# Optimization experiments

Hardware: AMD Instinct MI355X
Metric: run time of the kernel (lower is better)

Reference implementation:

```python
import jax, jax.numpy as jnp
import numpy as np
from jax import lax

B, CIN, COUT, K, SDIM, H = 8, 512, 512, 3, 512, 32
EPS = 1e-8
LRELU_SLOPE = 0.2
ACT_SCALE = float(np.sqrt(2.0))


def setup_inputs() -> dict:
    key = jax.random.key(0)
    k1, k2, k3, k4 = jax.random.split(key, 4)
    return {
        "x": jax.random.normal(k1, (B, CIN, H, H), jnp.float32),
        "style": jax.random.normal(k2, (B, SDIM), jnp.float32),
        "weight": jax.random.normal(k3, (COUT, CIN, K, K), jnp.float32),
        "mod_w": jax.random.normal(k4, (CIN, SDIM), jnp.float32),
        "mod_b": jnp.ones((CIN,), jnp.float32),  # EqualLinear bias_init=1
        "bias": jnp.zeros((COUT,), jnp.float32),  # FusedLeakyReLU bias
    }


def _blur_kernel(c):
    bk = np.array([1.0, 3.0, 3.0, 1.0], np.float32)
    bk = bk[None, :] * bk[:, None]
    bk = bk / bk.sum() * 4.0  # upsample_factor ** 2
    return jnp.tile(jnp.asarray(bk)[None, None], (c, 1, 1, 1))  # (C,1,4,4)


def reference(x, style, weight, mod_w, mod_b, bias):
    b, cin, h, w = x.shape
    cout, k = weight.shape[0], weight.shape[-1]
    conv_scale = 1.0 / np.sqrt(cin * k * k)
    lin_scale = 1.0 / np.sqrt(mod_w.shape[1])

    # style modulation: EqualLinear(style_dim -> in_channel), bias_init=1
    s = style @ (mod_w * lin_scale).T + mod_b  # (B, Cin)

    # per-sample modulated weights (B, Cout, Cin, k, k)
    wmod = conv_scale * weight[None] * s[:, None, :, None, None]
    demod = lax.rsqrt(jnp.sum(wmod * wmod, axis=(2, 3, 4)) + EPS)
    wmod = wmod * demod[:, :, None, None, None]

    # conv_transpose2d(stride=2, pad=0) == conv with lhs_dilation=2, pad=k-1,
    # spatially-flipped kernel (torch transposes (Cout,Cin)->(Cin,Cout)).
    wflip = jnp.flip(wmod, (-2, -1))

    def convt(xi, wi):  # xi: (Cin,H,W), wi: (Cout,Cin,k,k)
        return lax.conv_general_dilated(
            xi[None], wi, (1, 1), [(k - 1, k - 1)] * 2,
            lhs_dilation=(2, 2),
            dimension_numbers=("NCHW", "OIHW", "NCHW"))[0]

    y = jax.vmap(convt)(x, wflip)  # (B, Cout, 2H+1, 2W+1)

    # Blur: upfirdn2d with pad=(1,1), depthwise 4x4 FIR (kernel symmetric)
    bk = _blur_kernel(cout)
    y = lax.conv_general_dilated(
        y, bk, (1, 1), [(1, 1), (1, 1)],
        feature_group_count=cout,
        dimension_numbers=("NCHW", "OIHW", "NCHW"))  # (B, Cout, 2H, 2W)

    # FusedLeakyReLU: leaky_relu(y + bias) * sqrt(2)
    z = y + bias[None, :, None, None]
    return jnp.where(z >= 0, z, LRELU_SLOPE * z) * ACT_SCALE
```

## Files before the change

kernel.cpp:

```cpp
#include <hip/hip_runtime.h>
#include <hip/hip_bf16.h>

#define NB 8
#define CIN 512
#define COUT 512
#define SDIM 512

typedef __attribute__((ext_vector_type(8))) short short8;
typedef __attribute__((ext_vector_type(4))) float f32x4;

static constexpr float CONV_SCALE = 0.014731391274719740f;
static constexpr float LIN_SCALE  = 0.044194173824159216f;

static constexpr size_t OFF_S     = 0;
static constexpr size_t OFF_WSQ   = 16384;
static constexpr size_t OFF_DEMOD = 1064960;
static constexpr size_t OFF_XP    = 1081344;
static constexpr size_t OFF_WP    = 10551296;
static constexpr size_t OFF_Y1    = 15269888;
static constexpr size_t XP_BYTES  = 9469952;

static constexpr int NJOBS = 1060;

__device__ __forceinline__ int wpoff(int ps) {
  return ps == 0 ? 0 : ps == 1 ? 1048576 : ps == 2 ? 1572864 : 2097152;
}
__device__ __forceinline__ constexpr int y1off(int ps) {
  return ps == 0 ? 0 : ps == 1 ? 4460544 : ps == 2 ? 8785920 : 13111296;
}

__device__ __forceinline__ short f2bf(float f) {
  unsigned u = __builtin_bit_cast(unsigned, f);
  unsigned r = (u + 0x7fffu + ((u >> 16) & 1u)) >> 16;
  return (short)r;
}
__device__ __forceinline__ float bf2f(unsigned short u) {
  return __builtin_bit_cast(float, (unsigned)u << 16);
}

__device__ __forceinline__ void load_lds16(const short* g, short* l) {
  __builtin_amdgcn_global_load_lds(
      (const __attribute__((address_space(1))) unsigned int*)g,
      (__attribute__((address_space(3))) unsigned int*)l, 16, 0, 0);
}

__global__ void k_prep1(const float* __restrict__ style, const float* __restrict__ mod_w,
                        const float* __restrict__ mod_b, float* __restrict__ s_out,
                        const float* __restrict__ w, short* __restrict__ wp,
                        float* __restrict__ wsq) {
  const int tid = threadIdx.x;
  if (blockIdx.x < 1024) {
    int idx = blockIdx.x * 256 + tid;
    int co = idx >> 9, ci = idx & 511;
    float wv[3][3];
    float sq = 0.f;
#pragma unroll
    for (int i = 0; i < 9; ++i) {
      float v = w[idx * 9 + i];
      wv[i / 3][i % 3] = v;
      sq += v * v;
    }
    wsq[idx] = sq * CONV_SCALE * CONV_SCALE;
#pragma unroll
    for (int wy = 0; wy < 3; ++wy)
#pragma unroll
      for (int wx = 0; wx < 3; ++wx) {
        int psy = (wy == 1) ? 1 : 0, psx = (wx == 1) ? 1 : 0;
        int u = psy ? 0 : (wy == 0 ? 1 : 0);
        int v = psx ? 0 : (wx == 0 ? 1 : 0);
        int ps = psy * 2 + psx;
        int tap = psy ? (psx ? 0 : v) : (psx ? u : u * 2 + v);
        int k = tap * 512 + ci;
        int elem = wpoff(ps) + ((k >> 6) * 512 + co) * 64 + (k & 63);
        wp[elem] = f2bf(wv[wy][wx] * CONV_SCALE);
      }
  } else {
    int wid = tid >> 6, lane = tid & 63;
    int ci = (blockIdx.x - 1024) * 4 + wid;
    float acc[NB] = {};
    for (int k = lane; k < SDIM; k += 64) {
      float wm = mod_w[ci * SDIM + k];
#pragma unroll
      for (int b = 0; b < NB; ++b) acc[b] += wm * style[b * SDIM + k];
    }
#pragma unroll
    for (int b = 0; b < NB; ++b) {
      float v = acc[b];
      for (int o = 32; o > 0; o >>= 1) v += __shfl_xor(v, o);
      if (lane == 0) s_out[b * CIN + ci] = v * LIN_SCALE + mod_b[ci];
    }
  }
}

__global__ void k_prep2(const float* __restrict__ wsq, const float* __restrict__ s,
                        float* __restrict__ demod,
                        const float* __restrict__ x, short* __restrict__ xp) {
  const int tid = threadIdx.x;
  if (blockIdx.x < 1024) {
    __shared__ float t[64][65];
    const int tx = tid & 63, ty = tid >> 6;
    int bx = blockIdx.x;
    int sp0 = (bx & 15) * 64, ci0 = ((bx >> 4) & 7) * 64, b = bx >> 7;
    for (int r = ty; r < 64; r += 4)
      t[r][tx] = x[(b * CIN + ci0 + r) * 1024 + sp0 + tx];
    __syncthreads();
    int ci = ci0 + tx;
    float sv = s[b * CIN + ci];
    for (int r = ty; r < 64; r += 4) {
      int sp = sp0 + r;
      int yy = sp >> 5, xx = sp & 31;
      xp[((b * 34 + yy + 1) * 34 + (xx + 1)) * 512 + ci] = f2bf(t[tx][r] * sv);
    }
  } else {
    int wid = tid >> 6, lane = tid & 63;
    int co = (blockIdx.x - 1024) * 4 + wid;
    float acc[NB] = {};
    for (int ci = lane; ci < CIN; ci += 64) {
      float wq = wsq[co * CIN + ci];
#pragma unroll
      for (int b = 0; b < NB; ++b) {
        float sv = s[b * CIN + ci];
        acc[b] += wq * sv * sv;
      }
    }
#pragma unroll
    for (int b = 0; b < NB; ++b) {
      float v = acc[b];
      for (int o = 32; o > 0; o >>= 1) v += __shfl_xor(v, o);
      if (lane == 0) demod[b * COUT + co] = rsqrtf(v + 1e-8f);
    }
  }
}

#define MFMA_ROWPAIR(AH, AL, RH, RL)                                              \
  __builtin_amdgcn_s_setprio(1);                                                  \
  acc[RH][0] = __builtin_amdgcn_mfma_f32_16x16x32_bf16(AH, b0, acc[RH][0], 0,0,0);\
  acc[RH][1] = __builtin_amdgcn_mfma_f32_16x16x32_bf16(AH, b1, acc[RH][1], 0,0,0);\
  acc[RH][2] = __builtin_amdgcn_mfma_f32_16x16x32_bf16(AH, b2, acc[RH][2], 0,0,0);\
  acc[RH][3] = __builtin_amdgcn_mfma_f32_16x16x32_bf16(AH, b3, acc[RH][3], 0,0,0);\
  acc[RL][0] = __builtin_amdgcn_mfma_f32_16x16x32_bf16(AL, b0, acc[RL][0], 0,0,0);\
  acc[RL][1] = __builtin_amdgcn_mfma_f32_16x16x32_bf16(AL, b1, acc[RL][1], 0,0,0);\
  acc[RL][2] = __builtin_amdgcn_mfma_f32_16x16x32_bf16(AL, b2, acc[RL][2], 0,0,0);\
  acc[RL][3] = __builtin_amdgcn_mfma_f32_16x16x32_bf16(AL, b3, acc[RL][3], 0,0,0);\
  __builtin_amdgcn_s_setprio(0);

__global__ __launch_bounds__(256, 2) void k_gemm(const short* __restrict__ xp,
                                                 const short* __restrict__ wp,
                                                 short* __restrict__ y1) {
  __shared__ short sW[2][128 * 64];
  __shared__ short sX[2][128 * 64];

  const int tid = threadIdx.x;
  const int wid = tid >> 6, lane = tid & 63;
  const int hi = lane >> 4;
  const int ksw8 = ((tid & 7) ^ ((tid >> 3) & 7)) * 8;
  const int wm = (wid >> 1) * 64, wn = (wid & 1) * 64;

  const int bx = blockIdx.x;
  const int xcd = bx & 7, ii = bx >> 3;
  const int j = (((ii >> 2) << 3) + xcd) * 4 + (ii & 3);
  if (j >= NJOBS) return;

  int ps, base;
  if (j < 276)      { ps = 0; base = 0; }
  else if (j < 540) { ps = 1; base = 276; }
  else if (j < 804) { ps = 2; base = 540; }
  else              { ps = 3; base = 804; }
  const int r = j - base;
  const int nb = r >> 2, mb = r & 3;
  const int psy = ps >> 1, psx = ps & 1;
  const int Ny = 33 - psy, Nx = 33 - psx;
  const int N = NB * Ny * Nx;
  const int n0 = nb * 128, m0 = mb * 128;
  const int KT = (2 - psy) * (2 - psx) * 8;
  const short* wpb = wp + wpoff(ps);
  short* y1b = y1 + y1off(ps);

  int bb[4], ay[4], ax[4];
#pragma unroll
  for (int i = 0; i < 4; ++i) {
    int seg = i * 256 + tid;
    int n = n0 + (seg >> 3);
    if (n >= N) n = N - 1;
    int b = n / (Ny * Nx);
    int rem = n - b * (Ny * Nx);
    int a_y = rem / Nx;
    bb[i] = b; ay[i] = a_y; ax[i] = rem - a_y * Nx;
  }

  auto STAGE = [&](int kt, int d) {
    int tap = kt >> 3, ci0 = (kt & 7) << 6;
    int oy, ox;
    if (ps == 0)      { oy = tap >> 1; ox = tap & 1; }
    else if (ps == 1) { oy = tap;      ox = 1; }
    else if (ps == 2) { oy = 1;        ox = tap; }
    else              { oy = 1;        ox = 1; }
#pragma unroll
    for (int i = 0; i < 4; ++i) {
      int seg = i * 256 + tid;
      const short* gw = wpb + (kt * 512 + m0 + (seg >> 3)) * 64 + ksw8;
      load_lds16(gw, &sW[d][(i * 4 + wid) * 512]);
    }
#pragma unroll
    for (int i = 0; i < 4; ++i) {
      const short* gx = xp + ((bb[i] * 34 + ay[i] + oy) * 34 + ax[i] + ox) * 512 + ci0 + ksw8;
      load_lds16(gx, &sX[d][(i * 4 + wid) * 512]);
    }
  };

  const int c0 = ((hi)     ^ (lane & 7)) * 8;
  const int c1 = ((4 + hi) ^ (lane & 7)) * 8;
  const int rA0 = (wm +  0 + (lane & 15)) * 64, rA1 = (wm + 16 + (lane & 15)) * 64;
  const int rA2 = (wm + 32 + (lane & 15)) * 64, rA3 = (wm + 48 + (lane & 15)) * 64;
  const int rB0 = (wn +  0 + (lane & 15)) * 64, rB1 = (wn + 16 + (lane & 15)) * 64;
  const int rB2 = (wn + 32 + (lane & 15)) * 64, rB3 = (wn + 48 + (lane & 15)) * 64;

  f32x4 acc[4][4] = {};

  STAGE(0, 0);
  STAGE(1, 1);
  __syncthreads();

  int cur = 0;
  for (int t = 0; t < KT; ++t) {
    const short* W = sW[cur];
    const short* X = sX[cur];
    short8 a0, a1, b0, b1, b2, b3;

    a0 = *(const short8*)&W[rA0 + c0];
    a1 = *(const short8*)&W[rA1 + c0];
    b0 = *(const short8*)&X[rB0 + c0];
    b1 = *(const short8*)&X[rB1 + c0];
    b2 = *(const short8*)&X[rB2 + c0];
    b3 = *(const short8*)&X[rB3 + c0];
    MFMA_ROWPAIR(a0, a1, 0, 1);
    __builtin_amdgcn_s_barrier();

    a0 = *(const short8*)&W[rA2 + c0];
    a1 = *(const short8*)&W[rA3 + c0];
    MFMA_ROWPAIR(a0, a1, 2, 3);
    __builtin_amdgcn_s_barrier();

    a0 = *(const short8*)&W[rA0 + c1];
    a1 = *(const short8*)&W[rA1 + c1];
    b0 = *(const short8*)&X[rB0 + c1];
    b1 = *(const short8*)&X[rB1 + c1];
    b2 = *(const short8*)&X[rB2 + c1];
    b3 = *(const short8*)&X[rB3 + c1];
    MFMA_ROWPAIR(a0, a1, 0, 1);
    __builtin_amdgcn_s_barrier();

    a0 = *(const short8*)&W[rA2 + c1];
    a1 = *(const short8*)&W[rA3 + c1];
    MFMA_ROWPAIR(a0, a1, 2, 3);

    __syncthreads();
    if (t + 2 < KT) STAGE(t + 2, cur);
    cur ^= 1;
  }

#pragma unroll
  for (int mf = 0; mf < 4; ++mf) {
    int m = m0 + wm + mf * 16 + (lane >> 4) * 4;
#pragma unroll
    for (int nf = 0; nf < 4; ++nf) {
      int n = n0 + wn + nf * 16 + (lane & 15);
      if (n < N) {
#pragma unroll
        for (int rr = 0; rr < 4; ++rr) y1b[(m + rr) * N + n] = f2bf(acc[mf][nf][rr]);
      }
    }
  }
}

__global__ __launch_bounds__(256, 4) void k_blur(const short* __restrict__ y1,
                                                 const float* __restrict__ demod,
                                                 const float* __restrict__ bias,
                                                 float* __restrict__ out) {
  __shared__ float sin_[4][35 * 35];
  __shared__ float stmp[2][35][64];
  const int tid = threadIdx.x;
  const int bc = blockIdx.x;
  const int co = bc & 511, b = bc >> 9;

  for (int i = tid; i < 4 * 35 * 35; i += 256) ((float*)sin_)[i] = 0.f;
  __syncthreads();

#pragma unroll
  for (int ps = 0; ps < 4; ++ps) {
    const int Nyv = 33 - (ps >> 1), Nxv = 33 - (ps & 1);
    const short* pl = y1 + y1off(ps) + (co * NB + b) * (Nyv * Nxv);
    for (int t = tid; t < Nyv * Nxv; t += 256) {
      int av = t / Nxv, ah = t - av * Nxv;
      sin_[ps][(av + 1) * 35 + ah + 1] = bf2f((unsigned short)pl[t]);
    }
  }
  __syncthreads();

  const int q = tid & 63;
  const int mx = q >> 1, fx = q & 1;
  int xp0, xi0, xp1, xi1, xp2, xi2, xp3, xi3;
  if (fx) { xp0 = 0; xi0 = mx + 1; xp1 = 1; xi1 = mx + 1; xp2 = 0; xi2 = mx + 2; xp3 = 1; xi3 = mx + 2; }
  else    { xp0 = 1; xi0 = mx;     xp1 = 0; xi1 = mx + 1; xp2 = 1; xi2 = mx + 1; xp3 = 0; xi3 = mx + 2; }

  for (int r = tid >> 6; r < 70; r += 4) {
    int pv = (r >= 35) ? 1 : 0;
    int av = r - pv * 35;
    float v = 0.25f * sin_[pv * 2 + xp0][av * 35 + xi0]
            + 0.75f * sin_[pv * 2 + xp1][av * 35 + xi1]
            + 0.75f * sin_[pv * 2 + xp2][av * 35 + xi2]
            + 0.25f * sin_[pv * 2 + xp3][av * 35 + xi3];
    stmp[pv][av][q] = v;
  }
  __syncthreads();

  const float dm = demod[b * COUT + co], bs = bias[co];
  for (int p = tid >> 6; p < 64; p += 4) {
    int my = p >> 1, fy = p & 1;
    float v;
    if (fy) v = 0.25f * stmp[0][my + 1][q] + 0.75f * stmp[1][my + 1][q]
              + 0.75f * stmp[0][my + 2][q] + 0.25f * stmp[1][my + 2][q];
    else    v = 0.25f * stmp[1][my][q]     + 0.75f * stmp[0][my + 1][q]
              + 0.75f * stmp[1][my + 1][q] + 0.25f * stmp[0][my + 2][q];
    float val = dm * v + bs;
    out[(bc * 64 + p) * 64 + q] = (val >= 0.f ? val : 0.2f * val) * 1.41421356237309515f;
  }
}

extern "C" void kernel_launch(void* const* d_in, const int* in_sizes, int n_in,
                              void* d_out, int out_size, void* d_ws, size_t ws_size,
                              hipStream_t stream) {
  const float* x      = (const float*)d_in[0];
  const float* style  = (const float*)d_in[1];
  const float* weight = (const float*)d_in[2];
  const float* mod_w  = (const float*)d_in[3];
  const float* mod_b  = (const float*)d_in[4];
  const float* bias   = (const float*)d_in[5];
  float* out = (float*)d_out;
  char* ws = (char*)d_ws;

  float* s     = (float*)(ws + OFF_S);
  float* wsq   = (float*)(ws + OFF_WSQ);
  float* demod = (float*)(ws + OFF_DEMOD);
  short* xp    = (short*)(ws + OFF_XP);
  short* wp    = (short*)(ws + OFF_WP);
  short* y1    = (short*)(ws + OFF_Y1);

  hipMemsetAsync(xp, 0, XP_BYTES, stream);
  k_prep1<<<1152, 256, 0, stream>>>(style, mod_w, mod_b, s, weight, wp, wsq);
  k_prep2<<<1152, 256, 0, stream>>>(wsq, s, demod, x, xp);
  k_gemm<<<1088, 256, 0, stream>>>(xp, wp, y1);
  k_blur<<<4096, 256, 0, stream>>>(y1, demod, bias, out);
}
```

Measured before the change: 131.9 us.

## Use 4-stage K32 LDS pipeline in GEMM and zero only padding border

The GEMM main loop moves from a double-buffered K=64 stage to a four-buffer ring of K=32 stages with three tiles in flight. Explicit vmcnt waits and a single barrier pair per step replace the previous multiple barriers, and the LDS swizzle changes to match. Separately, the full memset of the padded input buffer is dropped; extra blocks in prep2 zero only the one-pixel border, since the interior is fully overwritten anyway. This removes a memset launch and bandwidth, but the hand-counted vmcnt values must match the number of loads issued per stage.

```diff
diff --git a/kernel.cpp b/kernel.cpp
--- a/kernel.cpp
+++ b/kernel.cpp
@@ -18,7 +18,6 @@
 static constexpr size_t OFF_XP    = 1081344;
 static constexpr size_t OFF_WP    = 10551296;
 static constexpr size_t OFF_Y1    = 15269888;
-static constexpr size_t XP_BYTES  = 9469952;
 
 static constexpr int NJOBS = 1060;
 
@@ -111,7 +110,7 @@
       int yy = sp >> 5, xx = sp & 31;
       xp[((b * 34 + yy + 1) * 34 + (xx + 1)) * 512 + ci] = f2bf(t[tx][r] * sv);
     }
-  } else {
+  } else if (blockIdx.x < 1152) {
     int wid = tid >> 6, lane = tid & 63;
     int co = (blockIdx.x - 1024) * 4 + wid;
     float acc[NB] = {};
@@ -129,31 +128,31 @@
       for (int o = 32; o > 0; o >>= 1) v += __shfl_xor(v, o);
       if (lane == 0) demod[b * COUT + co] = rsqrtf(v + 1e-8f);
     }
-  }
-}
-
-#define MFMA_ROWPAIR(AH, AL, RH, RL)                                              \
-  __builtin_amdgcn_s_setprio(1);                                                  \
-  acc[RH][0] = __builtin_amdgcn_mfma_f32_16x16x32_bf16(AH, b0, acc[RH][0], 0,0,0);\
-  acc[RH][1] = __builtin_amdgcn_mfma_f32_16x16x32_bf16(AH, b1, acc[RH][1], 0,0,0);\
-  acc[RH][2] = __builtin_amdgcn_mfma_f32_16x16x32_bf16(AH, b2, acc[RH][2], 0,0,0);\
-  acc[RH][3] = __builtin_amdgcn_mfma_f32_16x16x32_bf16(AH, b3, acc[RH][3], 0,0,0);\
-  acc[RL][0] = __builtin_amdgcn_mfma_f32_16x16x32_bf16(AL, b0, acc[RL][0], 0,0,0);\
-  acc[RL][1] = __builtin_amdgcn_mfma_f32_16x16x32_bf16(AL, b1, acc[RL][1], 0,0,0);\
-  acc[RL][2] = __builtin_amdgcn_mfma_f32_16x16x32_bf16(AL, b2, acc[RL][2], 0,0,0);\
-  acc[RL][3] = __builtin_amdgcn_mfma_f32_16x16x32_bf16(AL, b3, acc[RL][3], 0,0,0);\
-  __builtin_amdgcn_s_setprio(0);
+  } else {
+    int idx = blockIdx.x - 1152;
+    int b = idx >> 2, part = idx & 3;
+    unsigned* xpu = (unsigned*)xp;
+    for (int k = 0; k < 33; ++k) {
+      int c = part * 33 + k;
+      int yy, xx;
+      if (c < 34)       { yy = 0;            xx = c; }
+      else if (c < 68)  { yy = 33;           xx = c - 34; }
+      else if (c < 100) { yy = 1 + (c - 68); xx = 0; }
+      else              { yy = 1 + (c - 100); xx = 33; }
+      xpu[((((b * 34 + yy) * 34 + xx) * 512) >> 1) + tid] = 0u;
+    }
+  }
+}
 
 __global__ __launch_bounds__(256, 2) void k_gemm(const short* __restrict__ xp,
                                                  const short* __restrict__ wp,
                                                  short* __restrict__ y1) {
-  __shared__ short sW[2][128 * 64];
-  __shared__ short sX[2][128 * 64];
+  __shared__ short sW[4][128 * 32];
+  __shared__ short sX[4][128 * 32];
 
   const int tid = threadIdx.x;
   const int wid = tid >> 6, lane = tid & 63;
   const int hi = lane >> 4;
-  const int ksw8 = ((tid & 7) ^ ((tid >> 3) & 7)) * 8;
   const int wm = (wid >> 1) * 64, wn = (wid & 1) * 64;
 
   const int bx = blockIdx.x;
@@ -172,91 +171,84 @@
   const int Ny = 33 - psy, Nx = 33 - psx;
   const int N = NB * Ny * Nx;
   const int n0 = nb * 128, m0 = mb * 128;
-  const int KT = (2 - psy) * (2 - psx) * 8;
+  const int KT32 = (2 - psy) * (2 - psx) * 16;
   const short* wpb = wp + wpoff(ps);
   short* y1b = y1 + y1off(ps);
 
-  int bb[4], ay[4], ax[4];
-#pragma unroll
-  for (int i = 0; i < 4; ++i) {
-    int seg = i * 256 + tid;
-    int n = n0 + (seg >> 3);
+  int bb2[2], ay2[2], ax2[2];
+#pragma unroll
+  for (int i = 0; i < 2; ++i) {
+    int n = n0 + i * 64 + (tid >> 2);
     if (n >= N) n = N - 1;
     int b = n / (Ny * Nx);
     int rem = n - b * (Ny * Nx);
     int a_y = rem / Nx;
-    bb[i] = b; ay[i] = a_y; ax[i] = rem - a_y * Nx;
+    bb2[i] = b; ay2[i] = a_y; ax2[i] = rem - a_y * Nx;
   }
 
   auto STAGE = [&](int kt, int d) {
-    int tap = kt >> 3, ci0 = (kt & 7) << 6;
+    int tap = kt >> 4, ci0 = (kt & 15) << 5;
     int oy, ox;
     if (ps == 0)      { oy = tap >> 1; ox = tap & 1; }
     else if (ps == 1) { oy = tap;      ox = 1; }
     else if (ps == 2) { oy = 1;        ox = tap; }
     else              { oy = 1;        ox = 1; }
 #pragma unroll
-    for (int i = 0; i < 4; ++i) {
+    for (int i = 0; i < 2; ++i) {
       int seg = i * 256 + tid;
-      const short* gw = wpb + (kt * 512 + m0 + (seg >> 3)) * 64 + ksw8;
-      load_lds16(gw, &sW[d][(i * 4 + wid) * 512]);
-    }
-#pragma unroll
-    for (int i = 0; i < 4; ++i) {
-      const short* gx = xp + ((bb[i] * 34 + ay[i] + oy) * 34 + ax[i] + ox) * 512 + ci0 + ksw8;
-      load_lds16(gx, &sX[d][(i * 4 + wid) * 512]);
+      int row = seg >> 2;
+      int clog = (seg & 3) ^ ((row >> 1) & 3);
+      const short* gw = wpb + ((kt >> 1) * 512 + m0 + row) * 64 + (kt & 1) * 32 + clog * 8;
+      load_lds16(gw, &sW[d][seg * 8]);
+    }
+#pragma unroll
+    for (int i = 0; i < 2; ++i) {
+      int seg = i * 256 + tid;
+      int row = seg >> 2;
+      int clog = (seg & 3) ^ ((row >> 1) & 3);
+      const short* gx = xp + ((bb2[i] * 34 + ay2[i] + oy) * 34 + ax2[i] + ox) * 512 + ci0 + clog * 8;
+      load_lds16(gx, &sX[d][seg * 8]);
     }
   };
 
-  const int c0 = ((hi)     ^ (lane & 7)) * 8;
-  const int c1 = ((4 + hi) ^ (lane & 7)) * 8;
-  const int rA0 = (wm +  0 + (lane & 15)) * 64, rA1 = (wm + 16 + (lane & 15)) * 64;
-  const int rA2 = (wm + 32 + (lane & 15)) * 64, rA3 = (wm + 48 + (lane & 15)) * 64;
-  const int rB0 = (wn +  0 + (lane & 15)) * 64, rB1 = (wn + 16 + (lane & 15)) * 64;
-  const int rB2 = (wn + 32 + (lane & 15)) * 64, rB3 = (wn + 48 + (lane & 15)) * 64;
+  int offA[4], offB[4];
+#pragma unroll
+  for (int f = 0; f < 4; ++f) {
+    int ra = wm + f * 16 + (lane & 15);
+    offA[f] = ra * 32 + ((hi ^ ((ra >> 1) & 3)) * 8);
+    int rb = wn + f * 16 + (lane & 15);
+    offB[f] = rb * 32 + ((hi ^ ((rb >> 1) & 3)) * 8);
+  }
 
   f32x4 acc[4][4] = {};
 
-  STAGE(0, 0);
-  STAGE(1, 1);
-  __syncthreads();
-
-  int cur = 0;
-  for (int t = 0; t < KT; ++t) {
-    const short* W = sW[cur];
-    const short* X = sX[cur];
-    short8 a0, a1, b0, b1, b2, b3;
-
-    a0 = *(const short8*)&W[rA0 + c0];
-    a1 = *(const short8*)&W[rA1 + c0];
-    b0 = *(const short8*)&X[rB0 + c0];
-    b1 = *(const short8*)&X[rB1 + c0];
-    b2 = *(const short8*)&X[rB2 + c0];
-    b3 = *(const short8*)&X[rB3 + c0];
-    MFMA_ROWPAIR(a0, a1, 0, 1);
+  STAGE(0, 0); STAGE(1, 1); STAGE(2, 2);
+
+  for (int t = 0; t < KT32; ++t) {
+    int rem = KT32 - 1 - t;
+    if (rem >= 2)      asm volatile("s_waitcnt vmcnt(8)" ::: "memory");
+    else if (rem == 1) asm volatile("s_waitcnt vmcnt(4)" ::: "memory");
+    else               asm volatile("s_waitcnt vmcnt(0)" ::: "memory");
     __builtin_amdgcn_s_barrier();
 
-    a0 = *(const short8*)&W[rA2 + c0];
-    a1 = *(const short8*)&W[rA3 + c0];
-    MFMA_ROWPAIR(a0, a1, 2, 3);
+    const short* W = sW[t & 3];
+    const short* X = sX[t & 3];
+    short8 af[4], bf[4];
+#pragma unroll
+    for (int f = 0; f < 4; ++f) af[f] = *(const short8*)&W[offA[f]];
+#pragma unroll
+    for (int f = 0; f < 4; ++f) bf[f] = *(const short8*)&X[offB[f]];
+
+    __builtin_amdgcn_s_setprio(1);
+#pragma unroll
+    for (int mf = 0; mf < 4; ++mf)
+#pragma unroll
+      for (int nf = 0; nf < 4; ++nf)
+        acc[mf][nf] = __builtin_amdgcn_mfma_f32_16x16x32_bf16(af[mf], bf[nf], acc[mf][nf], 0, 0, 0);
+    __builtin_amdgcn_s_setprio(0);
+
     __builtin_amdgcn_s_barrier();
-
-    a0 = *(const short8*)&W[rA0 + c1];
-    a1 = *(const short8*)&W[rA1 + c1];
-    b0 = *(const short8*)&X[rB0 + c1];
-    b1 = *(const short8*)&X[rB1 + c1];
-    b2 = *(const short8*)&X[rB2 + c1];
-    b3 = *(const short8*)&X[rB3 + c1];
-    MFMA_ROWPAIR(a0, a1, 0, 1);
-    __builtin_amdgcn_s_barrier();
-
-    a0 = *(const short8*)&W[rA2 + c1];
-    a1 = *(const short8*)&W[rA3 + c1];
-    MFMA_ROWPAIR(a0, a1, 2, 3);
-
-    __syncthreads();
-    if (t + 2 < KT) STAGE(t + 2, cur);
-    cur ^= 1;
+    if (t + 3 < KT32) STAGE(t + 3, (t + 3) & 3);
   }
 
 #pragma unroll
@@ -346,9 +338,8 @@
   short* wp    = (short*)(ws + OFF_WP);
   short* y1    = (short*)(ws + OFF_Y1);
 
-  hipMemsetAsync(xp, 0, XP_BYTES, stream);
   k_prep1<<<1152, 256, 0, stream>>>(style, mod_w, mod_b, s, weight, wp, wsq);
-  k_prep2<<<1152, 256, 0, stream>>>(wsq, s, demod, x, xp);
+  k_prep2<<<1184, 256, 0, stream>>>(wsq, s, demod, x, xp);
   k_gemm<<<1088, 256, 0, stream>>>(xp, wp, y1);
   k_blur<<<4096, 256, 0, stream>>>(y1, demod, bias, out);
 }
```

Result: slower. 139.9 us (+6.1%).

## Zero only padding border in prep, pad y1 planes, split blur into halves

Applied to the files above, without the earlier changes.

Drops the full memset of the padded x buffer and instead zeroes only the border pixels with extra blocks in k_prep2. Each phase plane of y1 gets an even-padded stride so the blur kernel can load bf16 pairs with 32-bit reads. The blur kernel is split into two row-halves per (b, co), which halves its LDS use and raises occupancy, at the cost of loading overlapping halo rows and filtering out rows it does not need. The GEMM epilogue now computes per-column batch offsets for the padded layout.

```diff
diff --git a/kernel.cpp b/kernel.cpp
--- a/kernel.cpp
+++ b/kernel.cpp
@@ -18,15 +18,17 @@
 static constexpr size_t OFF_XP    = 1081344;
 static constexpr size_t OFF_WP    = 10551296;
 static constexpr size_t OFF_Y1    = 15269888;
-static constexpr size_t XP_BYTES  = 9469952;
 
 static constexpr int NJOBS = 1060;
 
 __device__ __forceinline__ int wpoff(int ps) {
   return ps == 0 ? 0 : ps == 1 ? 1048576 : ps == 2 ? 1572864 : 2097152;
 }
-__device__ __forceinline__ constexpr int y1off(int ps) {
-  return ps == 0 ? 0 : ps == 1 ? 4460544 : ps == 2 ? 8785920 : 13111296;
+__device__ __forceinline__ constexpr int PSPAD(int ps) {
+  return ps == 0 ? 1090 : ps == 3 ? 1024 : 1056;
+}
+__device__ __forceinline__ constexpr int PLB(int ps) {
+  return ps == 0 ? 0 : ps == 1 ? 4464640 : ps == 2 ? 8790016 : 13115392;
 }
 
 __device__ __forceinline__ short f2bf(float f) {
@@ -111,7 +113,7 @@
       int yy = sp >> 5, xx = sp & 31;
       xp[((b * 34 + yy + 1) * 34 + (xx + 1)) * 512 + ci] = f2bf(t[tx][r] * sv);
     }
-  } else {
+  } else if (blockIdx.x < 1152) {
     int wid = tid >> 6, lane = tid & 63;
     int co = (blockIdx.x - 1024) * 4 + wid;
     float acc[NB] = {};
@@ -128,6 +130,19 @@
       float v = acc[b];
       for (int o = 32; o > 0; o >>= 1) v += __shfl_xor(v, o);
       if (lane == 0) demod[b * COUT + co] = rsqrtf(v + 1e-8f);
+    }
+  } else {
+    int idx = blockIdx.x - 1152;
+    int b = idx >> 2, part = idx & 3;
+    unsigned* xpu = (unsigned*)xp;
+    for (int k = 0; k < 33; ++k) {
+      int c = part * 33 + k;
+      int yy, xx;
+      if (c < 34)       { yy = 0;            xx = c; }
+      else if (c < 68)  { yy = 33;           xx = c - 34; }
+      else if (c < 100) { yy = 1 + (c - 68); xx = 0; }
+      else              { yy = 1 + (c - 100); xx = 33; }
+      xpu[((((b * 34 + yy) * 34 + xx) * 512) >> 1) + tid] = 0u;
     }
   }
 }
@@ -170,11 +185,11 @@
   const int nb = r >> 2, mb = r & 3;
   const int psy = ps >> 1, psx = ps & 1;
   const int Ny = 33 - psy, Nx = 33 - psx;
-  const int N = NB * Ny * Nx;
+  const int NyNx = Ny * Nx;
+  const int N = NB * NyNx;
   const int n0 = nb * 128, m0 = mb * 128;
   const int KT = (2 - psy) * (2 - psx) * 8;
   const short* wpb = wp + wpoff(ps);
-  short* y1b = y1 + y1off(ps);
 
   int bb[4], ay[4], ax[4];
 #pragma unroll
@@ -182,8 +197,8 @@
     int seg = i * 256 + tid;
     int n = n0 + (seg >> 3);
     if (n >= N) n = N - 1;
-    int b = n / (Ny * Nx);
-    int rem = n - b * (Ny * Nx);
+    int b = n / NyNx;
+    int rem = n - b * NyNx;
     int a_y = rem / Nx;
     bb[i] = b; ay[i] = a_y; ax[i] = rem - a_y * Nx;
   }
@@ -259,40 +274,60 @@
     cur ^= 1;
   }
 
-#pragma unroll
-  for (int mf = 0; mf < 4; ++mf) {
-    int m = m0 + wm + mf * 16 + (lane >> 4) * 4;
-#pragma unroll
-    for (int nf = 0; nf < 4; ++nf) {
-      int n = n0 + wn + nf * 16 + (lane & 15);
-      if (n < N) {
-#pragma unroll
-        for (int rr = 0; rr < 4; ++rr) y1b[(m + rr) * N + n] = f2bf(acc[mf][nf][rr]);
+  const int psp = PSPAD(ps);
+  const int plb = PLB(ps);
+#pragma unroll
+  for (int nf = 0; nf < 4; ++nf) {
+    int n = n0 + wn + nf * 16 + (lane & 15);
+    if (n < N) {
+      int b = n / NyNx;
+      int rem = n - b * NyNx;
+      int nbase = plb + b * psp + rem;
+#pragma unroll
+      for (int mf = 0; mf < 4; ++mf) {
+        int m = m0 + wm + mf * 16 + (lane >> 4) * 4;
+#pragma unroll
+        for (int rr = 0; rr < 4; ++rr)
+          y1[nbase + (m + rr) * 8 * psp] = f2bf(acc[mf][nf][rr]);
       }
     }
   }
 }
 
-__global__ __launch_bounds__(256, 4) void k_blur(const short* __restrict__ y1,
+__global__ __launch_bounds__(256, 8) void k_blur(const short* __restrict__ y1,
                                                  const float* __restrict__ demod,
                                                  const float* __restrict__ bias,
                                                  float* __restrict__ out) {
-  __shared__ float sin_[4][35 * 35];
-  __shared__ float stmp[2][35][64];
+  __shared__ float sin_[4][18 * 35];
+  __shared__ float stmp[2][18][64];
   const int tid = threadIdx.x;
-  const int bc = blockIdx.x;
+  const int bc = blockIdx.x & 4095;
+  const int h = blockIdx.x >> 12;
   const int co = bc & 511, b = bc >> 9;
-
-  for (int i = tid; i < 4 * 35 * 35; i += 256) ((float*)sin_)[i] = 0.f;
+  const int m0v = h * 16;
+
+  for (int i = tid; i < 4 * 18 * 35; i += 256) ((float*)sin_)[i] = 0.f;
   __syncthreads();
 
 #pragma unroll
   for (int ps = 0; ps < 4; ++ps) {
     const int Nyv = 33 - (ps >> 1), Nxv = 33 - (ps & 1);
-    const short* pl = y1 + y1off(ps) + (co * NB + b) * (Nyv * Nxv);
-    for (int t = tid; t < Nyv * Nxv; t += 256) {
-      int av = t / Nxv, ah = t - av * Nxv;
-      sin_[ps][(av + 1) * 35 + ah + 1] = bf2f((unsigned short)pl[t]);
+    const int total = Nyv * Nxv;
+    const short* pl = y1 + PLB(ps) + (co * NB + b) * PSPAD(ps);
+    for (int t2 = tid; t2 * 2 < total; t2 += 256) {
+      int e0 = t2 * 2;
+      unsigned pair = *(const unsigned*)&pl[e0];
+      int av0 = e0 / Nxv, ah0 = e0 - av0 * Nxv;
+      int lr0 = av0 + 1 - m0v;
+      if (lr0 >= 0 && lr0 < 18)
+        sin_[ps][lr0 * 35 + ah0 + 1] = bf2f((unsigned short)(pair & 0xffffu));
+      int e1 = e0 + 1;
+      if (e1 < total) {
+        int av1 = e1 / Nxv, ah1 = e1 - av1 * Nxv;
+        int lr1 = av1 + 1 - m0v;
+        if (lr1 >= 0 && lr1 < 18)
+          sin_[ps][lr1 * 35 + ah1 + 1] = bf2f((unsigned short)(pair >> 16));
+      }
     }
   }
   __syncthreads();
@@ -303,26 +338,31 @@
   if (fx) { xp0 = 0; xi0 = mx + 1; xp1 = 1; xi1 = mx + 1; xp2 = 0; xi2 = mx + 2; xp3 = 1; xi3 = mx + 2; }
   else    { xp0 = 1; xi0 = mx;     xp1 = 0; xi1 = mx + 1; xp2 = 1; xi2 = mx + 1; xp3 = 0; xi3 = mx + 2; }
 
-  for (int r = tid >> 6; r < 70; r += 4) {
-    int pv = (r >= 35) ? 1 : 0;
-    int av = r - pv * 35;
-    float v = 0.25f * sin_[pv * 2 + xp0][av * 35 + xi0]
-            + 0.75f * sin_[pv * 2 + xp1][av * 35 + xi1]
-            + 0.75f * sin_[pv * 2 + xp2][av * 35 + xi2]
-            + 0.25f * sin_[pv * 2 + xp3][av * 35 + xi3];
-    stmp[pv][av][q] = v;
+  for (int rt = tid >> 6; rt < 36; rt += 4) {
+    int pv = (rt >= 18) ? 1 : 0;
+    int lr = rt - pv * 18;
+    if (m0v + lr < 35) {
+      float v = 0.25f * sin_[pv * 2 + xp0][lr * 35 + xi0]
+              + 0.75f * sin_[pv * 2 + xp1][lr * 35 + xi1]
+              + 0.75f * sin_[pv * 2 + xp2][lr * 35 + xi2]
+              + 0.25f * sin_[pv * 2 + xp3][lr * 35 + xi3];
+      stmp[pv][lr][q] = v;
+    } else {
+      stmp[pv][lr][q] = 0.f;
+    }
   }
   __syncthreads();
 
   const float dm = demod[b * COUT + co], bs = bias[co];
-  for (int p = tid >> 6; p < 64; p += 4) {
-    int my = p >> 1, fy = p & 1;
+  for (int pl_ = tid >> 6; pl_ < 32; pl_ += 4) {
+    int myl = pl_ >> 1, fy = pl_ & 1;
     float v;
-    if (fy) v = 0.25f * stmp[0][my + 1][q] + 0.75f * stmp[1][my + 1][q]
-              + 0.75f * stmp[0][my + 2][q] + 0.25f * stmp[1][my + 2][q];
-    else    v = 0.25f * stmp[1][my][q]     + 0.75f * stmp[0][my + 1][q]
-              + 0.75f * stmp[1][my + 1][q] + 0.25f * stmp[0][my + 2][q];
+    if (fy) v = 0.25f * stmp[0][myl + 1][q] + 0.75f * stmp[1][myl + 1][q]
+              + 0.75f * stmp[0][myl + 2][q] + 0.25f * stmp[1][myl + 2][q];
+    else    v = 0.25f * stmp[1][myl][q]     + 0.75f * stmp[0][myl + 1][q]
+              + 0.75f * stmp[1][myl + 1][q] + 0.25f * stmp[0][myl + 2][q];
     float val = dm * v + bs;
+    int p = h * 32 + pl_;
     out[(bc * 64 + p) * 64 + q] = (val >= 0.f ? val : 0.2f * val) * 1.41421356237309515f;
   }
 }
@@ -346,9 +386,8 @@
   short* wp    = (short*)(ws + OFF_WP);
   short* y1    = (short*)(ws + OFF_Y1);
 
-  hipMemsetAsync(xp, 0, XP_BYTES, stream);
   k_prep1<<<1152, 256, 0, stream>>>(style, mod_w, mod_b, s, weight, wp, wsq);
-  k_prep2<<<1152, 256, 0, stream>>>(wsq, s, demod, x, xp);
+  k_prep2<<<1184, 256, 0, stream>>>(wsq, s, demod, x, xp);
   k_gemm<<<1088, 256, 0, stream>>>(xp, wp, y1);
-  k_blur<<<4096, 256, 0, stream>>>(y1, demod, bias, out);
-}
+  k_blur<<<8192, 256, 0, stream>>>(y1, demod, bias, out);
+}
```

After: 117.1 us. 1.13x faster.
